# Performance work log

Measured on AMD Instinct MI355X. Metric: run time of the kernel, lower is better.

## Reference

```python
import jax, jax.numpy as jnp
import numpy as np

STRIDES = (8, 16, 32)
NUM_CLASSES = 80
BINS = 16
TOPK = 10
W_CLS, W_IOU, W_DFL = 0.5, 7.5, 1.5
EPS = 1e-9


def make_grid(H, W, stride):
    ys, xs = jnp.meshgrid(jnp.arange(H, dtype=jnp.float32),
                          jnp.arange(W, dtype=jnp.float32), indexing='ij')
    return jnp.stack([(xs + 0.5) * stride, (ys + 0.5) * stride], -1).reshape(-1, 2)


def decode_dfl(dfl, grid, stride):
    # dfl: (B, 64, H, W), channel layout coord-major (4 coords x 16 bins)
    B, C, H, W = dfl.shape
    prob = jax.nn.softmax(dfl.reshape(B, 4, BINS, H, W), axis=2)
    proj = jnp.arange(BINS, dtype=dfl.dtype)
    dist = jnp.einsum('bkchw,c->bkhw', prob, proj)              # expected bin value
    dist = dist.transpose(0, 2, 3, 1).reshape(B, H * W, 4) * stride  # (B,N,4) ltrb px
    cx, cy = grid[:, 0], grid[:, 1]
    return jnp.stack([cx - dist[..., 0], cy - dist[..., 1],
                      cx + dist[..., 2], cy + dist[..., 3]], -1)   # (B,N,4) xyxy


def pairwise_iou(gt, pr, eps=1e-7):
    # gt (B,G,4), pr (B,N,4) -> (B,G,N)
    lt = jnp.maximum(gt[:, :, None, :2], pr[:, None, :, :2])
    rb = jnp.minimum(gt[:, :, None, 2:], pr[:, None, :, 2:])
    wh = jnp.clip(rb - lt, 0.0)
    inter = wh[..., 0] * wh[..., 1]
    ag = jnp.clip(gt[..., 2] - gt[..., 0], 0) * jnp.clip(gt[..., 3] - gt[..., 1], 0)
    ap = jnp.clip(pr[..., 2] - pr[..., 0], 0) * jnp.clip(pr[..., 3] - pr[..., 1], 0)
    return inter / (ag[:, :, None] + ap[:, None, :] - inter + eps)


def ciou(b1, b2, eps=1e-7):
    # elementwise CIoU over (...,4) xyxy boxes
    w1, h1 = b1[..., 2] - b1[..., 0], b1[..., 3] - b1[..., 1]
    w2, h2 = b2[..., 2] - b2[..., 0], b2[..., 3] - b2[..., 1]
    lt = jnp.maximum(b1[..., :2], b2[..., :2])
    rb = jnp.minimum(b1[..., 2:], b2[..., 2:])
    wh = jnp.clip(rb - lt, 0.0)
    inter = wh[..., 0] * wh[..., 1]
    union = w1 * h1 + w2 * h2 - inter + eps
    iou = inter / union
    cw = jnp.maximum(b1[..., 2], b2[..., 2]) - jnp.minimum(b1[..., 0], b2[..., 0])
    ch = jnp.maximum(b1[..., 3], b2[..., 3]) - jnp.minimum(b1[..., 1], b2[..., 1])
    c2 = cw * cw + ch * ch + eps
    rho2 = ((b1[..., 0] + b1[..., 2] - b2[..., 0] - b2[..., 2]) ** 2 +
            (b1[..., 1] + b1[..., 3] - b2[..., 1] - b2[..., 3]) ** 2) / 4.0
    v = (4.0 / np.pi ** 2) * (jnp.arctan(w2 / (h2 + eps)) - jnp.arctan(w1 / (h1 + eps))) ** 2
    a = jax.lax.stop_gradient(v / (v - iou + (1.0 + eps)))
    return iou - rho2 / c2 - a * v


def tal_assign(scores, pred_boxes, gt_bboxes, gt_labels, grid, topk=TOPK, alpha=0.5, beta=6.0):
    B, N, C = scores.shape
    G = gt_bboxes.shape[1]
    mask_gt = gt_bboxes.sum(-1) > 0                                    # (B,G) zero-padded gts
    cx, cy = grid[None, None, :, 0], grid[None, None, :, 1]
    in_gts = ((cx > gt_bboxes[..., 0:1]) & (cx < gt_bboxes[..., 2:3]) &
              (cy > gt_bboxes[..., 1:2]) & (cy < gt_bboxes[..., 3:4]))  # (B,G,N)
    iou = pairwise_iou(gt_bboxes, pred_boxes)                          # (B,G,N)
    probs = jax.nn.sigmoid(scores)                                     # (B,N,C)
    idx = jnp.broadcast_to(gt_labels[:, None, :], (B, N, G))
    cls_g = jnp.take_along_axis(probs, idx, axis=2).transpose(0, 2, 1)  # (B,G,N)
    valid = in_gts & mask_gt[:, :, None]
    align = jnp.where(valid, (cls_g ** alpha) * (iou ** beta), 0.0)
    vals, idxk = jax.lax.top_k(align, topk)                            # (B,G,K)
    bi = jnp.arange(B)[:, None, None]
    gi = jnp.arange(G)[None, :, None]
    topk_mask = jnp.zeros((B, G, N), bool).at[bi, gi, idxk].set(vals > EPS)
    mask_pos = topk_mask & valid
    # resolve anchors assigned to multiple gts: keep gt with highest IoU
    multi = mask_pos.sum(1) > 1                                        # (B,N)
    best_gt = jnp.argmax(iou, axis=1)                                  # (B,N)
    best_oh = best_gt[:, None, :] == jnp.arange(G)[None, :, None]      # (B,G,N)
    mask_pos = jnp.where(multi[:, None, :], best_oh, mask_pos)
    fg_mask = mask_pos.any(1)                                          # (B,N)
    matched = jnp.argmax(mask_pos, axis=1)                             # (B,N)
    matched_gt_inds = jnp.where(fg_mask, matched, -1)
    target_bboxes = jnp.take_along_axis(gt_bboxes, matched[:, :, None], axis=1)
    target_labels = jnp.take_along_axis(gt_labels, matched, axis=1)
    t1h = jax.nn.one_hot(target_labels, C, dtype=scores.dtype) * fg_mask[..., None]
    align_pos = align * mask_pos
    pos_align_max = align_pos.max(2, keepdims=True)                    # per-gt max metric
    pos_iou_max = (iou * mask_pos).max(2, keepdims=True)               # per-gt max overlap
    norm = (align_pos * pos_iou_max / (pos_align_max + EPS)).max(1)    # (B,N)
    target_scores = t1h * norm[..., None]
    return target_scores, target_bboxes, fg_mask, matched_gt_inds


def yolo_loss(p0, p1, p2, gt_bboxes, gt_labels):
    scores_l, dfl_l, boxes_l, grids_l = [], [], [], []
    for p, s in zip((p0, p1, p2), STRIDES):
        B, _, H, W = p.shape
        N = H * W
        dfl, cls = p[:, :64], p[:, 64:64 + NUM_CLASSES]
        grid = make_grid(H, W, s)
        boxes_l.append(decode_dfl(dfl, grid, s))
        scores_l.append(cls.transpose(0, 2, 3, 1).reshape(B, N, NUM_CLASSES))
        dfl_l.append(dfl.transpose(0, 2, 3, 1).reshape(B, N, 4, BINS))
        grids_l.append(grid)
    all_scores = jnp.concatenate(scores_l, 1)      # (B,Nt,80)
    all_dfl = jnp.concatenate(dfl_l, 1)            # (B,Nt,4,16)
    pred_boxes = jnp.concatenate(boxes_l, 1)       # (B,Nt,4)
    grid = jnp.concatenate(grids_l, 0)             # (Nt,2)
    t_scores, t_boxes, fg, matched = tal_assign(all_scores, pred_boxes, gt_bboxes, gt_labels, grid)
    fgf = fg.astype(all_scores.dtype)
    num_pos = jnp.maximum(fgf.sum(), 1.0)
    # BCE with logits, stable form, soft targets
    s = all_scores
    bce = jnp.clip(s, 0.0) - s * t_scores + jnp.log1p(jnp.exp(-jnp.abs(s)))
    loss_cls = bce.sum() / num_pos
    loss_iou = ((1.0 - ciou(pred_boxes, t_boxes)) * fgf).sum() / num_pos  # mean over positives
    # DFL soft targets (original calls _make_dfl_targets with stride=1)
    m = jnp.clip(matched, 0)
    boxes = jnp.take_along_axis(gt_bboxes, m[:, :, None], axis=1)         # (B,Nt,4)
    gcx, gcy = grid[None, :, 0], grid[None, :, 1]
    dists = jnp.stack([jnp.clip(gcx - boxes[..., 0], 0.0),
                       jnp.clip(gcy - boxes[..., 1], 0.0),
                       jnp.clip(boxes[..., 2] - gcx, 0.0),
                       jnp.clip(boxes[..., 3] - gcy, 0.0)], -1)           # (B,Nt,4)
    tb = jnp.clip(dists, 0.0, BINS - 1 - 1e-6)
    lo = jnp.floor(tb)
    a = tb - lo
    li = lo.astype(jnp.int32)
    ui = jnp.minimum(li + 1, BINS - 1)
    td = (jax.nn.one_hot(li, BINS, dtype=tb.dtype) * (1.0 - a)[..., None] +
          jax.nn.one_hot(ui, BINS, dtype=tb.dtype) * a[..., None])        # (B,Nt,4,16)
    td = td * fgf[:, :, None, None]
    lsm = jax.nn.log_softmax(all_dfl, axis=-1)
    loss_dfl = -(td * lsm).sum() / num_pos
    return jnp.stack([W_IOU * loss_iou, W_CLS * loss_cls, W_DFL * loss_dfl])


def setup_inputs() -> dict:
    key = jax.random.key(0)
    k = jax.random.split(key, 6)
    B, G = 32, 32
    p0 = jax.random.normal(k[0], (B, 144, 80, 80), jnp.float32)
    p1 = jax.random.normal(k[1], (B, 144, 40, 40), jnp.float32)
    p2 = jax.random.normal(k[2], (B, 144, 20, 20), jnp.float32)
    c = jax.random.uniform(k[3], (B, G, 2), minval=60.0, maxval=580.0)
    wh = jax.random.uniform(k[4], (B, G, 2), minval=20.0, maxval=200.0)
    gt_bboxes = jnp.concatenate([jnp.clip(c - wh / 2, 0.0, 640.0),
                                 jnp.clip(c + wh / 2, 0.0, 640.0)], -1)
    gt_labels = jax.random.randint(k[5], (B, G), 0, NUM_CLASSES)
    return {'p0': p0, 'p1': p1, 'p2': p2, 'gt_bboxes': gt_bboxes, 'gt_labels': gt_labels}


def reference(p0, p1, p2, gt_bboxes, gt_labels):
    return yolo_loss(p0, p1, p2, gt_bboxes, gt_labels)
```

## Files before the change

kernel.cpp:

```cpp
#include <hip/hip_runtime.h>
#include <hip/hip_bf16.h>

#define NB 32
#define NG 32
#define NC 80
#define NTOT 8400
#define CH 144
#define BN (NB * NTOT)

#define TILES_PER_B 132
#define NBLK1 (NB * TILES_PER_B)
#define NBLKN 33
#define NBLK3 (NBLKN * NB)

struct AInfo {
    const float* base;
    int hw;
    int off;
    float cx, cy, stride;
};

__device__ __forceinline__ AInfo anchor_info(int n, int b, const float* p0, const float* p1, const float* p2) {
    AInfo ai;
    if (n < 6400) {
        int x = n % 80, y = n / 80;
        ai.hw = 6400; ai.off = n;
        ai.cx = (x + 0.5f) * 8.0f; ai.cy = (y + 0.5f) * 8.0f; ai.stride = 8.0f;
        ai.base = p0 + (size_t)b * CH * 6400;
    } else if (n < 8000) {
        int m = n - 6400; int x = m % 40, y = m / 40;
        ai.hw = 1600; ai.off = m;
        ai.cx = (x + 0.5f) * 16.0f; ai.cy = (y + 0.5f) * 16.0f; ai.stride = 16.0f;
        ai.base = p1 + (size_t)b * CH * 1600;
    } else {
        int m = n - 8000; int x = m % 20, y = m / 20;
        ai.hw = 400; ai.off = m;
        ai.cx = (x + 0.5f) * 32.0f; ai.cy = (y + 0.5f) * 32.0f; ai.stride = 32.0f;
        ai.base = p2 + (size_t)b * CH * 400;
    }
    return ai;
}

__device__ __forceinline__ void ins10(float a[10], float v) {
    if (v > a[9]) {
        a[9] = v;
#pragma unroll
        for (int i = 8; i >= 0; i--) {
            if (a[i + 1] > a[i]) { float t = a[i]; a[i] = a[i + 1]; a[i + 1] = t; }
        }
    }
}

__device__ __forceinline__ float iou_fn(float4 gb, float4 pb, float ap) {
    float ag = fmaxf(gb.z - gb.x, 0.f) * fmaxf(gb.w - gb.y, 0.f);
    float iw = fmaxf(fminf(gb.z, pb.z) - fmaxf(gb.x, pb.x), 0.f);
    float ih = fmaxf(fminf(gb.w, pb.w) - fmaxf(gb.y, pb.y), 0.f);
    float inter = iw * ih;
    return inter / (ag + ap - inter + 1e-7f);
}

__device__ __forceinline__ float align_metric(float s, float iou) {
    float sg = 1.f / (1.f + __expf(-s));
    float i2 = iou * iou;
    return sqrtf(sg) * i2 * i2 * i2;
}

__device__ __forceinline__ float ciou_fn(float4 p, float4 t) {
    float w1 = p.z - p.x, h1 = p.w - p.y;
    float w2 = t.z - t.x, h2 = t.w - t.y;
    float iw = fmaxf(fminf(p.z, t.z) - fmaxf(p.x, t.x), 0.f);
    float ih = fmaxf(fminf(p.w, t.w) - fmaxf(p.y, t.y), 0.f);
    float inter = iw * ih;
    float un = w1 * h1 + w2 * h2 - inter + 1e-7f;
    float iou = inter / un;
    float cw = fmaxf(p.z, t.z) - fminf(p.x, t.x);
    float chh = fmaxf(p.w, t.w) - fminf(p.y, t.y);
    float c2 = cw * cw + chh * chh + 1e-7f;
    float dx = p.x + p.z - t.x - t.z, dy = p.y + p.w - t.y - t.w;
    float rho2 = (dx * dx + dy * dy) * 0.25f;
    float da = atanf(w2 / (h2 + 1e-7f)) - atanf(w1 / (h1 + 1e-7f));
    float v = 0.4052847345693511f * da * da;
    float al = v / (v - iou + 1.f + 1e-7f);
    return iou - rho2 / c2 - al * v;
}

__global__ __launch_bounds__(256) void k1_fused(
    const float* __restrict__ p0, const float* __restrict__ p1, const float* __restrict__ p2,
    float* __restrict__ pred, float* __restrict__ lse, float* __restrict__ part_bce,
    float* __restrict__ posA, float* __restrict__ posI) {
    int blk = blockIdx.x;
    if (blk == 0) {
        for (int i = threadIdx.x; i < NB * NG; i += 256) { posA[i] = 0.f; posI[i] = 0.f; }
    }
    int b = blk / TILES_PER_B;
    int tile = blk - b * TILES_PER_B;
    const float* base; int hw, o0, lvl_off, W; float spx;
    if (tile < 100)      { base = p0; hw = 6400; o0 = tile * 64;          lvl_off = 0;    W = 80; spx = 8.f;  }
    else if (tile < 125) { base = p1; hw = 1600; o0 = (tile - 100) * 64;  lvl_off = 6400; W = 40; spx = 16.f; }
    else                 { base = p2; hw = 400;  o0 = (tile - 125) * 64;  lvl_off = 8000; W = 20; spx = 32.f; }
    base += (size_t)b * CH * hw;
    int valid = min(64, hw - o0);

    int a = threadIdx.x >> 2, k = threadIdx.x & 3;
    if (a < valid) {
        const float* col = base + (size_t)(k * 16) * hw + o0 + a;
        float v[16]; float mx = -1e30f;
#pragma unroll
        for (int j = 0; j < 16; j++) v[j] = col[(size_t)j * hw];
#pragma unroll
        for (int j = 0; j < 16; j++) mx = fmaxf(mx, v[j]);
        float se = 0.f, we = 0.f;
#pragma unroll
        for (int j = 0; j < 16; j++) { float e = __expf(v[j] - mx); se += e; we += e * (float)j; }
        float dist = we / se * spx;
        float lv = mx + __logf(se);
        int nl = o0 + a;
        int x = nl % W, y = nl / W;
        float cx = (x + 0.5f) * spx, cy = (y + 0.5f) * spx;
        float c = (k & 1) ? cy : cx;
        size_t ai = (size_t)b * NTOT + lvl_off + nl;
        pred[ai * 4 + k] = (k < 2) ? (c - dist) : (c + dist);
        lse[ai * 4 + k] = lv;
    }

    int valid4 = valid >> 2;
    const float* clsb = base + (size_t)64 * hw + o0;
    float4 vv[5]; bool okf[5];
#pragma unroll
    for (int i = 0; i < 5; i++) {
        int u = threadIdx.x + 256 * i;
        int ch = u >> 4, f4 = u & 15;
        okf[i] = (f4 < valid4);
        if (okf[i]) vv[i] = ((const float4*)(clsb + (size_t)ch * hw))[f4];
    }
    float bce = 0.f;
#pragma unroll
    for (int i = 0; i < 5; i++) {
        if (okf[i]) {
            float s;
            s = vv[i].x; bce += fmaxf(s, 0.f) + __logf(1.f + __expf(-fabsf(s)));
            s = vv[i].y; bce += fmaxf(s, 0.f) + __logf(1.f + __expf(-fabsf(s)));
            s = vv[i].z; bce += fmaxf(s, 0.f) + __logf(1.f + __expf(-fabsf(s)));
            s = vv[i].w; bce += fmaxf(s, 0.f) + __logf(1.f + __expf(-fabsf(s)));
        }
    }
#pragma unroll
    for (int off = 32; off > 0; off >>= 1) bce += __shfl_xor(bce, off, 64);
    __shared__ float red[4];
    if ((threadIdx.x & 63) == 0) red[threadIdx.x >> 6] = bce;
    __syncthreads();
    if (threadIdx.x == 0)
        part_bce[blk] = red[0] + red[1] + red[2] + red[3];
}

__global__ __launch_bounds__(256) void k2_thr(
    const float* __restrict__ p0, const float* __restrict__ p1, const float* __restrict__ p2,
    const float* __restrict__ gtb, const int* __restrict__ gtl,
    const float* __restrict__ pred, float* __restrict__ thr) {
    int g = blockIdx.x, b = blockIdx.y;
    const float* gb = gtb + (size_t)(b * NG + g) * 4;
    float gx1 = gb[0], gy1 = gb[1], gx2 = gb[2], gy2 = gb[3];
    bool vg = (gx1 + gy1 + gx2 + gy2) > 0.f;
    int label = gtl[b * NG + g];
    float4 gb4 = { gx1, gy1, gx2, gy2 };
    const float* bases[3] = { p0 + (size_t)b * CH * 6400,
                              p1 + (size_t)b * CH * 1600,
                              p2 + (size_t)b * CH * 400 };
    const int Ws[3] = { 80, 40, 20 }, hws[3] = { 6400, 1600, 400 }, loff[3] = { 0, 6400, 8000 };
    const float ss[3] = { 8.f, 16.f, 32.f };
    int X0[3], W_[3], Y0[3], CNT[3];
    int tot = 0;
#pragma unroll
    for (int l = 0; l < 3; l++) {
        int x0 = 0, x1 = -1, y0 = 0, y1 = -1;
        if (vg) {
            float s = ss[l];
            x0 = max(0, (int)floorf(gx1 / s - 0.5f));
            x1 = min(Ws[l] - 1, (int)floorf(gx2 / s - 0.5f) + 1);
            y0 = max(0, (int)floorf(gy1 / s - 0.5f));
            y1 = min(Ws[l] - 1, (int)floorf(gy2 / s - 0.5f) + 1);
        }
        int w = x1 - x0 + 1, h = y1 - y0 + 1;
        X0[l] = x0; Y0[l] = y0; W_[l] = w;
        CNT[l] = (w > 0 && h > 0) ? w * h : 0;
        tot += CNT[l];
    }
    float top[10];
#pragma unroll
    for (int i = 0; i < 10; i++) top[i] = 0.f;
    const float4* pred4 = (const float4*)pred + (size_t)b * NTOT;
    for (int i = threadIdx.x; i < tot; i += 256) {
        int l = 0, r = i;
        if (r >= CNT[0]) { r -= CNT[0]; l = 1; if (r >= CNT[1]) { r -= CNT[1]; l = 2; } }
        int w = W_[l];
        int y = Y0[l] + r / w, x = X0[l] + r % w;
        float s = ss[l];
        float cx = (x + 0.5f) * s, cy = (y + 0.5f) * s;
        int nr = y * Ws[l] + x;
        float4 pb = pred4[loff[l] + nr];
        float sc = bases[l][(size_t)(64 + label) * hws[l] + nr];
        float ap = fmaxf(pb.z - pb.x, 0.f) * fmaxf(pb.w - pb.y, 0.f);
        float iou = iou_fn(gb4, pb, ap);
        bool ing = (cx > gx1) && (cx < gx2) && (cy > gy1) && (cy < gy2);
        float al = 0.f;
        if (ing && vg) al = align_metric(sc, iou);
        ins10(top, al);
    }
    __shared__ float s_top[256 * 10];
#pragma unroll
    for (int i = 0; i < 10; i++) s_top[threadIdx.x * 10 + i] = top[i];
    __syncthreads();
    if (threadIdx.x < 64) {
        float mt[10];
#pragma unroll
        for (int i = 0; i < 10; i++) mt[i] = 0.f;
        for (int src = threadIdx.x; src < 256; src += 64)
#pragma unroll
            for (int i = 0; i < 10; i++) ins10(mt, s_top[src * 10 + i]);
        float thrv = 0.f;
        for (int r = 0; r < 10; r++) {
            unsigned long long key = ((unsigned long long)__float_as_uint(mt[0]) << 32) | (unsigned)threadIdx.x;
#pragma unroll
            for (int off = 32; off > 0; off >>= 1) {
                unsigned long long o = __shfl_xor(key, off, 64);
                if (o > key) key = o;
            }
            thrv = __uint_as_float((unsigned)(key >> 32));
            if ((key & 63ULL) == (unsigned long long)threadIdx.x) {
#pragma unroll
                for (int i = 0; i < 9; i++) mt[i] = mt[i + 1];
                mt[9] = 0.f;
            }
        }
        if (threadIdx.x == 0) thr[b * NG + g] = thrv;
    }
}

__global__ __launch_bounds__(256) void k3_mask(
    const float* __restrict__ p0, const float* __restrict__ p1, const float* __restrict__ p2,
    const float* __restrict__ thr, const float* __restrict__ pred,
    const float* __restrict__ gtb, const int* __restrict__ gtl,
    unsigned* __restrict__ maskv, int* __restrict__ matchedv,
    float* __restrict__ posA, float* __restrict__ posI, unsigned* __restrict__ partN) {
    int b = blockIdx.y;
    int n = blockIdx.x * 256 + threadIdx.x;
    __shared__ float s_thr[NG];
    __shared__ float4 s_gt[NG];
    __shared__ int s_lab[NG];
    if (threadIdx.x < NG) {
        s_thr[threadIdx.x] = thr[b * NG + threadIdx.x];
        float4 gb4 = ((const float4*)gtb)[b * NG + threadIdx.x];
        if (!((gb4.x + gb4.y + gb4.z + gb4.w) > 0.f))
            gb4 = make_float4(1e30f, 1e30f, -1e30f, -1e30f);
        s_gt[threadIdx.x] = gb4;
        s_lab[threadIdx.x] = gtl[b * NG + threadIdx.x];
    }
    __syncthreads();
    bool fg = false;
    if (n < NTOT) {
        AInfo ai = anchor_info(n, b, p0, p1, p2);
        float4 pb = ((const float4*)pred)[(size_t)b * NTOT + n];
        float ap = fmaxf(pb.z - pb.x, 0.f) * fmaxf(pb.w - pb.y, 0.f);
        unsigned m = 0;
        for (int g = 0; g < NG; g++) {
            float4 gb4 = s_gt[g];
            bool ing = (ai.cx > gb4.x) && (ai.cx < gb4.z) && (ai.cy > gb4.y) && (ai.cy < gb4.w);
            if (__any(ing)) {
                float al = 0.f;
                if (ing) {
                    float iou = iou_fn(gb4, pb, ap);
                    float s = ai.base[(size_t)(64 + s_lab[g]) * ai.hw + ai.off];
                    al = align_metric(s, iou);
                }
                if (al >= s_thr[g] && al > 1e-9f) m |= (1u << g);
            }
        }
        int cnt = __popc(m);
        int matched = -1;
        if (cnt > 0) {
            if (cnt > 1) {
                float best = -1.f; int bg = 0;
                for (int g = 0; g < NG; g++) {
                    float iou = iou_fn(s_gt[g], pb, ap);
                    if (iou > best) { best = iou; bg = g; }
                }
                m = 1u << bg;
            }
            for (int g = 0; g < NG; g++) {
                if ((m >> g) & 1u) {
                    float4 gb4 = s_gt[g];
                    float iou = iou_fn(gb4, pb, ap);
                    bool ing = (ai.cx > gb4.x) && (ai.cx < gb4.z) && (ai.cy > gb4.y) && (ai.cy < gb4.w);
                    float al = 0.f;
                    if (ing) {
                        float s = ai.base[(size_t)(64 + s_lab[g]) * ai.hw + ai.off];
                        al = align_metric(s, iou);
                    }
                    atomicMax((int*)&posI[b * NG + g], __float_as_int(iou));
                    atomicMax((int*)&posA[b * NG + g], __float_as_int(al));
                }
            }
            matched = __ffs(m) - 1;
            fg = true;
        }
        maskv[(size_t)b * NTOT + n] = m;
        matchedv[(size_t)b * NTOT + n] = matched;
    }
    unsigned long long bal = __ballot(fg);
    __shared__ unsigned redN[4];
    if ((threadIdx.x & 63) == 0) redN[threadIdx.x >> 6] = (unsigned)__popcll(bal);
    __syncthreads();
    if (threadIdx.x == 0)
        partN[blockIdx.y * gridDim.x + blockIdx.x] = redN[0] + redN[1] + redN[2] + redN[3];
}

__global__ __launch_bounds__(256) void k5_loss(
    const float* __restrict__ p0, const float* __restrict__ p1, const float* __restrict__ p2,
    const unsigned* __restrict__ maskv, const int* __restrict__ matchedv,
    const float* __restrict__ posA, const float* __restrict__ posI,
    const float* __restrict__ gtb, const int* __restrict__ gtl,
    const float* __restrict__ pred, const float* __restrict__ lse,
    float* __restrict__ part_corr, float* __restrict__ part_liou, float* __restrict__ part_ldfl) {
    int b = blockIdx.y;
    int n = blockIdx.x * 256 + threadIdx.x;
    __shared__ float4 s_gt[NG];
    __shared__ int s_lab[NG];
    __shared__ float s_pa[NG], s_pi[NG];
    if (threadIdx.x < NG) {
        s_gt[threadIdx.x] = ((const float4*)gtb)[b * NG + threadIdx.x];
        s_lab[threadIdx.x] = gtl[b * NG + threadIdx.x];
        s_pa[threadIdx.x] = posA[b * NG + threadIdx.x];
        s_pi[threadIdx.x] = posI[b * NG + threadIdx.x];
    }
    __syncthreads();
    float corr = 0.f, liou = 0.f, ldfl = 0.f;
    if (n < NTOT) {
        int mt = matchedv[(size_t)b * NTOT + n];
        if (mt >= 0) {
            AInfo ai = anchor_info(n, b, p0, p1, p2);
            const float* base = ai.base + ai.off;
            float4 pb = ((const float4*)pred)[(size_t)b * NTOT + n];
            float ap = fmaxf(pb.z - pb.x, 0.f) * fmaxf(pb.w - pb.y, 0.f);
            unsigned m = maskv[(size_t)b * NTOT + n];
            float nrm = 0.f;
            unsigned mm = m;
            while (mm) {
                int g = __ffs(mm) - 1; mm &= mm - 1;
                float4 gb4 = s_gt[g];
                float iou = iou_fn(gb4, pb, ap);
                bool ing = (ai.cx > gb4.x) && (ai.cx < gb4.z) && (ai.cy > gb4.y) && (ai.cy < gb4.w);
                float al = 0.f;
                if (ing) {
                    float s = base[(size_t)(64 + s_lab[g]) * ai.hw];
                    al = align_metric(s, iou);
                }
                nrm = fmaxf(nrm, al * s_pi[g] / (s_pa[g] + 1e-9f));
            }
            float s = base[(size_t)(64 + s_lab[mt]) * ai.hw];
            corr = s * nrm;
            float4 tb = s_gt[mt];
            liou = 1.f - ciou_fn(pb, tb);
            float4 l4 = ((const float4*)lse)[(size_t)b * NTOT + n];
            float lv[4] = { l4.x, l4.y, l4.z, l4.w };
            float d[4] = { fmaxf(ai.cx - tb.x, 0.f), fmaxf(ai.cy - tb.y, 0.f),
                           fmaxf(tb.z - ai.cx, 0.f), fmaxf(tb.w - ai.cy, 0.f) };
            float Ls[8];
            int li4[4], ui4[4]; float afr4[4];
#pragma unroll
            for (int k = 0; k < 4; k++) {
                float tbk = fminf(d[k], 14.999999f);
                float lo = floorf(tbk);
                afr4[k] = tbk - lo;
                li4[k] = (int)lo;
                ui4[k] = min(li4[k] + 1, 15);
            }
#pragma unroll
            for (int k = 0; k < 4; k++) {
                Ls[k * 2]     = base[(size_t)(k * 16 + li4[k]) * ai.hw];
                Ls[k * 2 + 1] = base[(size_t)(k * 16 + ui4[k]) * ai.hw];
            }
#pragma unroll
            for (int k = 0; k < 4; k++)
                ldfl += lv[k] - ((1.f - afr4[k]) * Ls[k * 2] + afr4[k] * Ls[k * 2 + 1]);
        }
    }
#pragma unroll
    for (int off = 32; off > 0; off >>= 1) {
        corr += __shfl_xor(corr, off, 64);
        liou += __shfl_xor(liou, off, 64);
        ldfl += __shfl_xor(ldfl, off, 64);
    }
    __shared__ float rc[4], ri[4], rd[4];
    if ((threadIdx.x & 63) == 0) {
        int w = threadIdx.x >> 6;
        rc[w] = corr; ri[w] = liou; rd[w] = ldfl;
    }
    __syncthreads();
    if (threadIdx.x == 0) {
        int blk = blockIdx.y * gridDim.x + blockIdx.x;
        part_corr[blk] = rc[0] + rc[1] + rc[2] + rc[3];
        part_liou[blk] = ri[0] + ri[1] + ri[2] + ri[3];
        part_ldfl[blk] = rd[0] + rd[1] + rd[2] + rd[3];
    }
}

__global__ __launch_bounds__(256) void k6_final(
    const float* __restrict__ part_bce, const float* __restrict__ part_corr,
    const float* __restrict__ part_liou, const float* __restrict__ part_ldfl,
    const unsigned* __restrict__ partN, float* __restrict__ out) {
    double bce = 0.0, corr = 0.0, liou = 0.0, ldfl = 0.0, np = 0.0;
    for (int i = threadIdx.x; i < NBLK1; i += 256) bce += (double)part_bce[i];
    for (int i = threadIdx.x; i < NBLK3; i += 256) {
        corr += (double)part_corr[i];
        liou += (double)part_liou[i];
        ldfl += (double)part_ldfl[i];
        np   += (double)partN[i];
    }
#pragma unroll
    for (int off = 32; off > 0; off >>= 1) {
        bce  += __shfl_xor(bce, off, 64);
        corr += __shfl_xor(corr, off, 64);
        liou += __shfl_xor(liou, off, 64);
        ldfl += __shfl_xor(ldfl, off, 64);
        np   += __shfl_xor(np, off, 64);
    }
    __shared__ double rb[4], rc[4], ri[4], rd[4], rn[4];
    if ((threadIdx.x & 63) == 0) {
        int w = threadIdx.x >> 6;
        rb[w] = bce; rc[w] = corr; ri[w] = liou; rd[w] = ldfl; rn[w] = np;
    }
    __syncthreads();
    if (threadIdx.x == 0) {
        bce  = rb[0] + rb[1] + rb[2] + rb[3];
        corr = rc[0] + rc[1] + rc[2] + rc[3];
        liou = ri[0] + ri[1] + ri[2] + ri[3];
        ldfl = rd[0] + rd[1] + rd[2] + rd[3];
        np   = rn[0] + rn[1] + rn[2] + rn[3];
        if (np < 1.0) np = 1.0;
        out[0] = (float)(7.5 * liou / np);
        out[1] = (float)(0.5 * (bce - corr) / np);
        out[2] = (float)(1.5 * ldfl / np);
    }
}

extern "C" void kernel_launch(void* const* d_in, const int* in_sizes, int n_in,
                              void* d_out, int out_size, void* d_ws, size_t ws_size,
                              hipStream_t stream) {
    const float* p0 = (const float*)d_in[0];
    const float* p1 = (const float*)d_in[1];
    const float* p2 = (const float*)d_in[2];
    const float* gtb = (const float*)d_in[3];
    const int* gtl = (const int*)d_in[4];
    float* out = (float*)d_out;

    char* w = (char*)d_ws;
    float* pred = (float*)w;
    float* lse = pred + (size_t)BN * 4;
    float* thr = lse + (size_t)BN * 4;
    float* posA = thr + NB * NG;
    float* posI = posA + NB * NG;
    unsigned* maskv = (unsigned*)(posI + NB * NG);
    int* matchedv = (int*)(maskv + BN);
    float* part_bce = (float*)(matchedv + BN);
    float* part_corr = part_bce + NBLK1;
    float* part_liou = part_corr + NBLK3;
    float* part_ldfl = part_liou + NBLK3;
    unsigned* partN = (unsigned*)(part_ldfl + NBLK3);

    hipLaunchKernelGGL(k1_fused, dim3(NBLK1), dim3(256), 0, stream,
                       p0, p1, p2, pred, lse, part_bce, posA, posI);
    hipLaunchKernelGGL(k2_thr, dim3(NG, NB), dim3(256), 0, stream,
                       p0, p1, p2, gtb, gtl, pred, thr);
    hipLaunchKernelGGL(k3_mask, dim3(NBLKN, NB), dim3(256), 0, stream,
                       p0, p1, p2, thr, pred, gtb, gtl, maskv, matchedv, posA, posI, partN);
    hipLaunchKernelGGL(k5_loss, dim3(NBLKN, NB), dim3(256), 0, stream,
                       p0, p1, p2, maskv, matchedv, posA, posI, gtb, gtl, pred, lse,
                       part_corr, part_liou, part_ldfl);
    hipLaunchKernelGGL(k6_final, dim3(1), dim3(256), 0, stream,
                       part_bce, part_corr, part_liou, part_ldfl, partN, out);
}
```

Baseline: 249.5 us.

## Widen k1 tiles to 256 anchors with float4 loads per thread

The fused decode/BCE kernel now covers 256 anchors per block instead of 64, so it launches about a quarter as many blocks. Each thread loads float4 vectors across 16 DFL bins and computes softmax for four anchors at once. The class-logit BCE pass is restructured so each wave walks 20 channels with float4 loads in two batches of ten. This targets per-block overhead and scalar load inefficiency, at the cost of more registers per thread and fewer blocks to spread across the GPU.

```diff
diff --git a/kernel.cpp b/kernel.cpp
--- a/kernel.cpp
+++ b/kernel.cpp
@@ -8,7 +8,7 @@
 #define CH 144
 #define BN (NB * NTOT)
 
-#define TILES_PER_B 132
+#define TILES_PER_B 34
 #define NBLK1 (NB * TILES_PER_B)
 #define NBLKN 33
 #define NBLK3 (NBLKN * NB)
@@ -84,6 +84,15 @@
     return iou - rho2 / c2 - al * v;
 }
 
+__device__ __forceinline__ float softplus4(float4 v) {
+    float r = 0.f, s;
+    s = v.x; r += fmaxf(s, 0.f) + __logf(1.f + __expf(-fabsf(s)));
+    s = v.y; r += fmaxf(s, 0.f) + __logf(1.f + __expf(-fabsf(s)));
+    s = v.z; r += fmaxf(s, 0.f) + __logf(1.f + __expf(-fabsf(s)));
+    s = v.w; r += fmaxf(s, 0.f) + __logf(1.f + __expf(-fabsf(s)));
+    return r;
+}
+
 __global__ __launch_bounds__(256) void k1_fused(
     const float* __restrict__ p0, const float* __restrict__ p1, const float* __restrict__ p2,
     float* __restrict__ pred, float* __restrict__ lse, float* __restrict__ part_bce,
@@ -95,54 +104,61 @@
     int b = blk / TILES_PER_B;
     int tile = blk - b * TILES_PER_B;
     const float* base; int hw, o0, lvl_off, W; float spx;
-    if (tile < 100)      { base = p0; hw = 6400; o0 = tile * 64;          lvl_off = 0;    W = 80; spx = 8.f;  }
-    else if (tile < 125) { base = p1; hw = 1600; o0 = (tile - 100) * 64;  lvl_off = 6400; W = 40; spx = 16.f; }
-    else                 { base = p2; hw = 400;  o0 = (tile - 125) * 64;  lvl_off = 8000; W = 20; spx = 32.f; }
+    if (tile < 25)      { base = p0; hw = 6400; o0 = tile * 256;        lvl_off = 0;    W = 80; spx = 8.f;  }
+    else if (tile < 32) { base = p1; hw = 1600; o0 = (tile - 25) * 256; lvl_off = 6400; W = 40; spx = 16.f; }
+    else                { base = p2; hw = 400;  o0 = (tile - 32) * 256; lvl_off = 8000; W = 20; spx = 32.f; }
     base += (size_t)b * CH * hw;
-    int valid = min(64, hw - o0);
-
-    int a = threadIdx.x >> 2, k = threadIdx.x & 3;
-    if (a < valid) {
-        const float* col = base + (size_t)(k * 16) * hw + o0 + a;
-        float v[16]; float mx = -1e30f;
-#pragma unroll
-        for (int j = 0; j < 16; j++) v[j] = col[(size_t)j * hw];
-#pragma unroll
-        for (int j = 0; j < 16; j++) mx = fmaxf(mx, v[j]);
-        float se = 0.f, we = 0.f;
-#pragma unroll
-        for (int j = 0; j < 16; j++) { float e = __expf(v[j] - mx); se += e; we += e * (float)j; }
-        float dist = we / se * spx;
-        float lv = mx + __logf(se);
-        int nl = o0 + a;
-        int x = nl % W, y = nl / W;
-        float cx = (x + 0.5f) * spx, cy = (y + 0.5f) * spx;
-        float c = (k & 1) ? cy : cx;
-        size_t ai = (size_t)b * NTOT + lvl_off + nl;
-        pred[ai * 4 + k] = (k < 2) ? (c - dist) : (c + dist);
-        lse[ai * 4 + k] = lv;
-    }
-
+    int valid = min(256, hw - o0);
     int valid4 = valid >> 2;
-    const float* clsb = base + (size_t)64 * hw + o0;
-    float4 vv[5]; bool okf[5];
-#pragma unroll
-    for (int i = 0; i < 5; i++) {
-        int u = threadIdx.x + 256 * i;
-        int ch = u >> 4, f4 = u & 15;
-        okf[i] = (f4 < valid4);
-        if (okf[i]) vv[i] = ((const float4*)(clsb + (size_t)ch * hw))[f4];
-    }
+    int hw4 = hw >> 2, o04 = o0 >> 2;
+    const float4* base4 = (const float4*)base;
+
+    int g4 = threadIdx.x >> 2, k = threadIdx.x & 3;
+    if (g4 < valid4) {
+        float4 v[16];
+#pragma unroll
+        for (int j = 0; j < 16; j++)
+            v[j] = base4[(size_t)(k * 16 + j) * hw4 + o04 + g4];
+        float dist[4], lv[4];
+#pragma unroll
+        for (int c = 0; c < 4; c++) {
+            float mx = -1e30f;
+#pragma unroll
+            for (int j = 0; j < 16; j++) { float x = ((const float*)&v[j])[c]; mx = fmaxf(mx, x); }
+            float se = 0.f, we = 0.f;
+#pragma unroll
+            for (int j = 0; j < 16; j++) {
+                float e = __expf(((const float*)&v[j])[c] - mx);
+                se += e; we += e * (float)j;
+            }
+            dist[c] = we / se * spx;
+            lv[c] = mx + __logf(se);
+        }
+#pragma unroll
+        for (int c = 0; c < 4; c++) {
+            int nl = o0 + g4 * 4 + c;
+            int x = nl % W, y = nl / W;
+            float cx = (x + 0.5f) * spx, cy = (y + 0.5f) * spx;
+            float ctr = (k & 1) ? cy : cx;
+            size_t ai = (size_t)b * NTOT + lvl_off + nl;
+            pred[ai * 4 + k] = (k < 2) ? (ctr - dist[c]) : (ctr + dist[c]);
+            lse[ai * 4 + k] = lv[c];
+        }
+    }
+
+    int wv = threadIdx.x >> 6, f4 = threadIdx.x & 63;
     float bce = 0.f;
-#pragma unroll
-    for (int i = 0; i < 5; i++) {
-        if (okf[i]) {
-            float s;
-            s = vv[i].x; bce += fmaxf(s, 0.f) + __logf(1.f + __expf(-fabsf(s)));
-            s = vv[i].y; bce += fmaxf(s, 0.f) + __logf(1.f + __expf(-fabsf(s)));
-            s = vv[i].z; bce += fmaxf(s, 0.f) + __logf(1.f + __expf(-fabsf(s)));
-            s = vv[i].w; bce += fmaxf(s, 0.f) + __logf(1.f + __expf(-fabsf(s)));
-        }
+    if (f4 < valid4) {
+        const float4* clsb = base4 + (size_t)64 * hw4 + o04 + f4;
+        float4 vv[10];
+#pragma unroll
+        for (int i = 0; i < 10; i++) vv[i] = clsb[(size_t)(wv + i * 4) * hw4];
+#pragma unroll
+        for (int i = 0; i < 10; i++) bce += softplus4(vv[i]);
+#pragma unroll
+        for (int i = 0; i < 10; i++) vv[i] = clsb[(size_t)(wv + (i + 10) * 4) * hw4];
+#pragma unroll
+        for (int i = 0; i < 10; i++) bce += softplus4(vv[i]);
     }
 #pragma unroll
     for (int off = 32; off > 0; off >>= 1) bce += __shfl_xor(bce, off, 64);
```

After: 253.9 us. Within noise of the previous version (+1.8%).
